# Kernel optimization log

Hardware: AMD Instinct MI355X
Metric: run time of the kernel (lower is better)

## Reference

```python
import jax, jax.numpy as jnp
import numpy as np

B, S, D = 1, 2048, 4096
H, KV, HD = 32, 8, 128
REP = H // KV            # 4, GQA repeat factor
THETA = 500000.0
NEG = -1e9               # stand-in for -inf in additive causal mask


def _rope(x, cos, sin):
    # x: [B,S,h,HD]; complex rotation on interleaved (even,odd) pairs,
    # matching torch.view_as_complex on [..., HD/2, 2]
    xr, xi = x[..., 0::2], x[..., 1::2]
    c = cos[None, :, None, :]
    s = sin[None, :, None, :]
    out_r = xr * c - xi * s
    out_i = xr * s + xi * c
    return jnp.stack([out_r, out_i], axis=-1).reshape(x.shape)


def setup_inputs() -> dict:
    key = jax.random.key(0)
    ks = jax.random.split(key, 6)
    x = jax.random.normal(ks[0], (B, S, D), dtype=jnp.float32)
    # torch nn.Linear weights are [out, in]
    sc = 1.0 / np.sqrt(D)
    wq = jax.random.normal(ks[1], (H * HD, D), dtype=jnp.float32) * sc
    wk = jax.random.normal(ks[2], (KV * HD, D), dtype=jnp.float32) * sc
    wv = jax.random.normal(ks[3], (KV * HD, D), dtype=jnp.float32) * sc
    wo = jax.random.normal(ks[4], (D, H * HD), dtype=jnp.float32) * sc
    # RoPE freqs_cis = exp(i * t * theta_f), stored as cos/sin [S, HD/2]
    freqs = 1.0 / (THETA ** (jnp.arange(0, HD, 2, dtype=jnp.float32) / HD))
    ang = jnp.outer(jnp.arange(S, dtype=jnp.float32), freqs)
    cos, sin = jnp.cos(ang), jnp.sin(ang)
    cache = jnp.zeros((2, B, S, KV, HD), dtype=jnp.float32)
    mask = jnp.where(jnp.tril(jnp.ones((S, S), dtype=bool)), 0.0, NEG).astype(jnp.float32)
    return {"x": x, "wq": wq, "wk": wk, "wv": wv, "wo": wo,
            "cos": cos, "sin": sin, "cache": cache, "mask": mask,
            "start_pos": 0}


def reference(x, wq, wk, wv, wo, cos, sin, cache, mask, start_pos):
    b, s, _ = x.shape
    xq = (x @ wq.T).reshape(b, s, H, HD)
    xk = (x @ wk.T).reshape(b, s, KV, HD)
    xv = (x @ wv.T).reshape(b, s, KV, HD)
    xq = _rope(xq, cos, sin)
    xk = _rope(xk, cos, sin)
    # functional KV-cache write
    cache = cache.at[0, :b, start_pos:start_pos + s].set(xk)
    cache = cache.at[1, :b, start_pos:start_pos + s].set(xv)
    keys = cache[0, :b, :start_pos + s]    # [b,T,KV,HD]
    values = cache[1, :b, :start_pos + s]  # [b,T,KV,HD]
    # GQA: head h = kv*REP + r (repeat_interleave ordering)
    q = xq.reshape(b, s, KV, REP, HD)
    scores = jnp.einsum('bskrd,btkd->bkrst', q, keys) / jnp.sqrt(jnp.float32(HD))
    scores = scores + mask[None, None, None]           # [b,KV,REP,s,T]
    p = jax.nn.softmax(scores.astype(jnp.float32), axis=-1).astype(x.dtype)
    out = jnp.einsum('bkrst,btkd->bskrd', p, values).reshape(b, s, H * HD)
    return out @ wo.T
```

## Files before the change

kernel.cpp:

```cpp
#include <hip/hip_runtime.h>
#include <stdint.h>

typedef __bf16 bf16_8 __attribute__((ext_vector_type(8)));
typedef __bf16 bf16_4 __attribute__((ext_vector_type(4)));
typedef float  f32x4  __attribute__((ext_vector_type(4)));

#define B_  1
#define S_  2048
#define D_  4096
#define H_  32
#define KV_ 8
#define HD_ 128

__device__ inline void gload_lds16(const void* g, void* l) {
  __builtin_amdgcn_global_load_lds((const __attribute__((address_space(1))) void*)g,
                                   (__attribute__((address_space(3))) void*)l, 16, 0, 0);
}

__global__ __launch_bounds__(256) void cvt_all(const float* __restrict__ x,
                                               const float* __restrict__ wq,
                                               const float* __restrict__ wk,
                                               const float* __restrict__ wv,
                                               const float* __restrict__ wo,
                                               __bf16* __restrict__ dst) {
  int i = blockIdx.x * 256 + threadIdx.x;
  const float* s;
  int j = i;
  if (j < 2097152) s = x;
  else if ((j -= 2097152) < 4194304) s = wq;
  else if ((j -= 4194304) < 1048576) s = wk;
  else if ((j -= 1048576) < 1048576) s = wv;
  else { j -= 1048576; s = wo; }
  float4 v = ((const float4*)s)[j];
  bf16_4 o = { (__bf16)v.x, (__bf16)v.y, (__bf16)v.z, (__bf16)v.w };
  ((bf16_4*)dst)[i] = o;
}

__global__ __launch_bounds__(256) void gemm_qkv(const __bf16* __restrict__ xb,
                                                const __bf16* __restrict__ wqb,
                                                const __bf16* __restrict__ wkb,
                                                const __bf16* __restrict__ wvb,
                                                const float* __restrict__ cosT,
                                                const float* __restrict__ sinT,
                                                __bf16* __restrict__ Qb,
                                                __bf16* __restrict__ Kb,
                                                __bf16* __restrict__ Vt) {
  __shared__ __bf16 As[128 * 32];
  __shared__ __bf16 Bs[128 * 32];
  const int nb = blockIdx.x, mb = blockIdx.y;
  const __bf16* W; int wrow0;
  if (nb < 32)      { W = wqb; wrow0 = nb * 128; }
  else if (nb < 40) { W = wkb; wrow0 = (nb - 32) * 128; }
  else              { W = wvb; wrow0 = (nb - 40) * 128; }
  const int tid = threadIdx.x, lane = tid & 63, wv = tid >> 6;
  const int wm = wv >> 1, wn = wv & 1;
  const int srow = lane >> 2, scol = (lane & 3) * 8;

  const __bf16* Ag0 = xb + (size_t)(mb * 128 + 2 * wv * 16 + srow) * D_ + scol;
  const __bf16* Bg0 = W  + (size_t)(wrow0 + 2 * wv * 16 + srow) * D_ + scol;
  __bf16* Al = As + 2 * wv * 512;
  __bf16* Bl = Bs + 2 * wv * 512;

  const f32x4 zv = {0.f, 0.f, 0.f, 0.f};
  f32x4 acc[4][4];
#pragma unroll
  for (int i = 0; i < 4; ++i)
#pragma unroll
    for (int j = 0; j < 4; ++j) acc[i][j] = zv;

  for (int k0 = 0; k0 < D_; k0 += 32) {
    gload_lds16(Ag0 + k0, Al);
    gload_lds16(Ag0 + (size_t)16 * D_ + k0, Al + 512);
    gload_lds16(Bg0 + k0, Bl);
    gload_lds16(Bg0 + (size_t)16 * D_ + k0, Bl + 512);
    __syncthreads();
    bf16_8 af[4], bfr[4];
#pragma unroll
    for (int i = 0; i < 4; ++i)
      af[i] = *(const bf16_8*)&As[(wm * 64 + i * 16 + (lane & 15)) * 32 + (lane >> 4) * 8];
#pragma unroll
    for (int j = 0; j < 4; ++j)
      bfr[j] = *(const bf16_8*)&Bs[(wn * 64 + j * 16 + (lane & 15)) * 32 + (lane >> 4) * 8];
#pragma unroll
    for (int i = 0; i < 4; ++i)
#pragma unroll
      for (int j = 0; j < 4; ++j)
        acc[i][j] = __builtin_amdgcn_mfma_f32_16x16x32_bf16(af[i], bfr[j], acc[i][j], 0, 0, 0);
    __syncthreads();
  }

#pragma unroll
  for (int i = 0; i < 4; ++i) {
    int row0 = mb * 128 + wm * 64 + i * 16 + (lane >> 4) * 4;
#pragma unroll
    for (int j = 0; j < 4; ++j) {
      int cl = wn * 64 + j * 16 + (lane & 15);
      if (nb < 40) {
        int f = cl >> 1;
        float sgn = (cl & 1) ? 1.f : -1.f;
        f32x4 v = acc[i][j];
        float o[4];
#pragma unroll
        for (int r = 0; r < 4; ++r) {
          float p = __shfl_xor(v[r], 1);
          float c = cosT[(size_t)(row0 + r) * 64 + f];
          float s = sinT[(size_t)(row0 + r) * 64 + f];
          o[r] = v[r] * c + sgn * p * s;
        }
        if (nb < 32) {
          int colg = nb * 128 + cl;
#pragma unroll
          for (int r = 0; r < 4; ++r)
            Qb[(size_t)(row0 + r) * D_ + colg] = (__bf16)o[r];
        } else {
          int colg = (nb - 32) * 128 + cl;
#pragma unroll
          for (int r = 0; r < 4; ++r)
            Kb[(size_t)(row0 + r) * 1024 + colg] = (__bf16)o[r];
        }
      } else {
        int colg = (nb - 40) * 128 + cl;
        bf16_4 pv = { (__bf16)acc[i][j][0], (__bf16)acc[i][j][1],
                      (__bf16)acc[i][j][2], (__bf16)acc[i][j][3] };
        *(bf16_4*)&Vt[(size_t)colg * S_ + row0] = pv;
      }
    }
  }
}

__global__ __launch_bounds__(256) void gemm_out(const __bf16* __restrict__ Ob,
                                                const __bf16* __restrict__ wob,
                                                float* __restrict__ Of) {
  __shared__ __bf16 As[128 * 32];
  __shared__ __bf16 Bs[128 * 32];
  const int nb = blockIdx.x, mb = blockIdx.y;
  const int tid = threadIdx.x, lane = tid & 63, wv = tid >> 6;
  const int wm = wv >> 1, wn = wv & 1;
  const int srow = lane >> 2, scol = (lane & 3) * 8;

  const __bf16* Ag0 = Ob  + (size_t)(mb * 128 + 2 * wv * 16 + srow) * D_ + scol;
  const __bf16* Bg0 = wob + (size_t)(nb * 128 + 2 * wv * 16 + srow) * D_ + scol;
  __bf16* Al = As + 2 * wv * 512;
  __bf16* Bl = Bs + 2 * wv * 512;

  const f32x4 zv = {0.f, 0.f, 0.f, 0.f};
  f32x4 acc[4][4];
#pragma unroll
  for (int i = 0; i < 4; ++i)
#pragma unroll
    for (int j = 0; j < 4; ++j) acc[i][j] = zv;

  for (int k0 = 0; k0 < D_; k0 += 32) {
    gload_lds16(Ag0 + k0, Al);
    gload_lds16(Ag0 + (size_t)16 * D_ + k0, Al + 512);
    gload_lds16(Bg0 + k0, Bl);
    gload_lds16(Bg0 + (size_t)16 * D_ + k0, Bl + 512);
    __syncthreads();
    bf16_8 af[4], bfr[4];
#pragma unroll
    for (int i = 0; i < 4; ++i)
      af[i] = *(const bf16_8*)&As[(wm * 64 + i * 16 + (lane & 15)) * 32 + (lane >> 4) * 8];
#pragma unroll
    for (int j = 0; j < 4; ++j)
      bfr[j] = *(const bf16_8*)&Bs[(wn * 64 + j * 16 + (lane & 15)) * 32 + (lane >> 4) * 8];
#pragma unroll
    for (int i = 0; i < 4; ++i)
#pragma unroll
      for (int j = 0; j < 4; ++j)
        acc[i][j] = __builtin_amdgcn_mfma_f32_16x16x32_bf16(af[i], bfr[j], acc[i][j], 0, 0, 0);
    __syncthreads();
  }

#pragma unroll
  for (int i = 0; i < 4; ++i) {
    int row0 = mb * 128 + wm * 64 + i * 16 + (lane >> 4) * 4;
#pragma unroll
    for (int j = 0; j < 4; ++j) {
      int colg = nb * 128 + wn * 64 + j * 16 + (lane & 15);
#pragma unroll
      for (int r = 0; r < 4; ++r)
        Of[(size_t)(row0 + r) * D_ + colg] = acc[i][j][r];
    }
  }
}

#define COMPUTE_TILE(ACC, MR, LR, AQ, QB0, DOMASK, KSB, VSB)                       \
  {                                                                                \
    f32x4 sfr_[4];                                                                 \
    __builtin_amdgcn_s_setprio(1);                                                 \
    _Pragma("unroll")                                                              \
    for (int nf = 0; nf < 4; ++nf) {                                               \
      f32x4 c_ = zv;                                                               \
      _Pragma("unroll")                                                            \
      for (int ks = 0; ks < 4; ++ks) {                                             \
        int n_ = nf * 16 + (lane & 15);                                            \
        int bo_ = (n_ * 256 + (ks * 32 + (lane >> 4) * 8) * 2) ^ ((n_ & 7) << 4);  \
        bf16_8 bk_ = *(const bf16_8*)((char*)(KSB) + bo_);                         \
        c_ = __builtin_amdgcn_mfma_f32_16x16x32_bf16(bk_, AQ[ks], c_, 0, 0, 0);    \
      }                                                                            \
      sfr_[nf] = c_;                                                               \
    }                                                                              \
    __builtin_amdgcn_s_setprio(0);                                                 \
    const int myq_ = (QB0) + w * 16 + (lane & 15);                                 \
    float pmn_[4];                                                                 \
    _Pragma("unroll")                                                              \
    for (int nf = 0; nf < 4; ++nf) {                                               \
      float t_ = -3e38f;                                                           \
      _Pragma("unroll")                                                            \
      for (int r = 0; r < 4; ++r) {                                                \
        int kcol_ = kb * 64 + nf * 16 + (lane >> 4) * 4 + r;                       \
        float v_ = sfr_[nf][r];                                                    \
        if ((DOMASK) && kcol_ > myq_) v_ = -1e9f;                                  \
        sfr_[nf][r] = v_;                                                          \
        t_ = fmaxf(t_, v_);                                                        \
      }                                                                            \
      pmn_[nf] = t_;                                                               \
    }                                                                              \
    float pm_ = fmaxf(fmaxf(pmn_[0], pmn_[1]), fmaxf(pmn_[2], pmn_[3]));           \
    pm_ = fmaxf(pm_, __shfl_xor(pm_, 16));                                         \
    pm_ = fmaxf(pm_, __shfl_xor(pm_, 32));                                         \
    if (!__all(pm_ <= MR + 8.f)) {                                                 \
      float mn_ = fmaxf(MR, pm_);                                                  \
      float rs_ = __expf(MR - mn_);                                                \
      MR = mn_;                                                                    \
      LR *= rs_;                                                                   \
      float rsb_[4];                                                               \
      _Pragma("unroll")                                                            \
      for (int r = 0; r < 4; ++r)                                                  \
        rsb_[r] = __shfl(rs_, (lane & 48) | ((lane >> 4) * 4 + r));                \
      _Pragma("unroll")                                                            \
      for (int d = 0; d < 8; ++d)                                                  \
        _Pragma("unroll")                                                          \
        for (int r = 0; r < 4; ++r) ACC[d][r] *= rsb_[r];                          \
    }                                                                              \
    float psn_[4];                                                                 \
    _Pragma("unroll")                                                              \
    for (int nf = 0; nf < 4; ++nf) {                                               \
      bf16_4 pk_;                                                                  \
      float t_ = 0.f;                                                              \
      _Pragma("unroll")                                                            \
      for (int r = 0; r < 4; ++r) {                                                \
        float p_ = __expf(sfr_[nf][r] - MR);                                       \
        t_ += p_;                                                                  \
        pk_[r] = (__bf16)p_;                                                       \
      }                                                                            \
      psn_[nf] = t_;                                                               \
      int bo_ = ((lane & 15) * 128 + nf * 32 + (lane >> 4) * 8) ^                  \
                (((lane & 15) & 7) << 4);                                          \
      *(bf16_4*)((char*)(&Ps[w][0]) + bo_) = pk_;                                  \
    }                                                                              \
    float ps_ = (psn_[0] + psn_[1]) + (psn_[2] + psn_[3]);                         \
    ps_ += __shfl_xor(ps_, 16);                                                    \
    ps_ += __shfl_xor(ps_, 32);                                                    \
    LR += ps_;                                                                     \
    bf16_8 ap_[2];                                                                 \
    _Pragma("unroll")                                                              \
    for (int ks = 0; ks < 2; ++ks) {                                               \
      int bo_ = ((lane & 15) * 128 + (ks * 32 + (lane >> 4) * 8) * 2) ^            \
                (((lane & 15) & 7) << 4);                                          \
      ap_[ks] = *(const bf16_8*)((char*)(&Ps[w][0]) + bo_);                        \
    }                                                                              \
    __builtin_amdgcn_s_setprio(1);                                                 \
    _Pragma("unroll")                                                              \
    for (int d = 0; d < 8; ++d) {                                                  \
      _Pragma("unroll")                                                            \
      for (int ks = 0; ks < 2; ++ks) {                                             \
        int dr_ = d * 16 + (lane & 15);                                            \
        int bo_ = (dr_ * 128 + (ks * 32 + (lane >> 4) * 8) * 2) ^ ((dr_ & 7) << 4);\
        bf16_8 bv_ = *(const bf16_8*)((char*)(VSB) + bo_);                         \
        ACC[d] = __builtin_amdgcn_mfma_f32_16x16x32_bf16(ap_[ks], bv_, ACC[d], 0, 0, 0); \
      }                                                                            \
    }                                                                              \
    __builtin_amdgcn_s_setprio(0);                                                 \
  }

__global__ __launch_bounds__(256) void attn_k(const __bf16* __restrict__ Qb,
                                              const __bf16* __restrict__ Kb,
                                              const __bf16* __restrict__ Vt,
                                              __bf16* __restrict__ Ob) {
  __shared__ __bf16 Ks[2][64 * 128];
  __shared__ __bf16 Vs[2][128 * 64];
  __shared__ __bf16 Ps[4][16 * 64];
  const int bid = blockIdx.x;
  const int kvh = bid & 7;
  const int j   = bid >> 3;
  const int h   = kvh * 4 + (j & 3);
  const int x   = j >> 2;
  const int qlo = x, qhi = 31 - x;
  const int tid = threadIdx.x, lane = tid & 63, w = tid >> 6;

  const float sc = 0.08838834764831845f;

  bf16_8 aq0[4], aq1[4];
#pragma unroll
  for (int ks = 0; ks < 4; ++ks) {
    int rr = w * 16 + (lane & 15);
    int cc = h * 128 + ks * 32 + (lane >> 4) * 8;
    bf16_8 t0 = *(const bf16_8*)&Qb[(size_t)(qlo * 64 + rr) * D_ + cc];
    bf16_8 t1 = *(const bf16_8*)&Qb[(size_t)(qhi * 64 + rr) * D_ + cc];
#pragma unroll
    for (int e = 0; e < 8; ++e) {
      aq0[ks][e] = (__bf16)((float)t0[e] * sc);
      aq1[ks][e] = (__bf16)((float)t1[e] * sc);
    }
  }

  const f32x4 zv = {0.f, 0.f, 0.f, 0.f};
  f32x4 accO0[8], accO1[8];
#pragma unroll
  for (int d = 0; d < 8; ++d) { accO0[d] = zv; accO1[d] = zv; }
  float mr0 = -3e38f, lr0 = 0.f, mr1 = -3e38f, lr1 = 0.f;

#define KSTAGE(BUF, KB)                                                            \
  {                                                                                \
    _Pragma("unroll")                                                              \
    for (int u = 0; u < 4; ++u) {                                                  \
      int chunk = (u * 4 + w) * 64 + lane;                                         \
      int row = chunk >> 4, p8 = chunk & 15;                                       \
      gload_lds16(&Kb[(size_t)((KB) * 64 + row) * 1024 + kvh * 128 + (p8 ^ (row & 7)) * 8], \
                  &Ks[BUF][(u * 4 + w) * 512]);                                    \
    }                                                                              \
    _Pragma("unroll")                                                              \
    for (int u = 0; u < 4; ++u) {                                                  \
      int chunk = (u * 4 + w) * 64 + lane;                                         \
      int vr = chunk >> 3, p8 = chunk & 7;                                         \
      gload_lds16(&Vt[(size_t)(kvh * 128 + vr) * S_ + (KB) * 64 + (p8 ^ (vr & 7)) * 8], \
                  &Vs[BUF][(u * 4 + w) * 512]);                                    \
    }                                                                              \
  }

  KSTAGE(0, 0);
  asm volatile("s_waitcnt vmcnt(0)" ::: "memory");
  __syncthreads();

  for (int kb = 0; kb <= qhi; ++kb) {
    const int cur = kb & 1;
    if (kb < qhi) KSTAGE(cur ^ 1, kb + 1);
    const __bf16* ksb = &Ks[cur][0];
    const __bf16* vsb = &Vs[cur][0];
    COMPUTE_TILE(accO1, mr1, lr1, aq1, qhi * 64, (kb == qhi), ksb, vsb);
    if (kb <= qlo) COMPUTE_TILE(accO0, mr0, lr0, aq0, qlo * 64, (kb == qlo), ksb, vsb);
    if (kb < qhi) {
      asm volatile("s_waitcnt vmcnt(0)" ::: "memory");
      __syncthreads();
    }
  }

  float inv0[4], inv1[4];
#pragma unroll
  for (int r = 0; r < 4; ++r) {
    int src = (lane & 48) | ((lane >> 4) * 4 + r);
    inv0[r] = 1.0f / __shfl(lr0, src);
    inv1[r] = 1.0f / __shfl(lr1, src);
  }
#pragma unroll
  for (int d = 0; d < 8; ++d) {
#pragma unroll
    for (int r = 0; r < 4; ++r) {
      size_t rl = (size_t)(qlo * 64 + w * 16 + (lane >> 4) * 4 + r);
      size_t rh = (size_t)(qhi * 64 + w * 16 + (lane >> 4) * 4 + r);
      int cc = h * 128 + d * 16 + (lane & 15);
      Ob[rl * D_ + cc] = (__bf16)(accO0[d][r] * inv0[r]);
      Ob[rh * D_ + cc] = (__bf16)(accO1[d][r] * inv1[r]);
    }
  }
}

extern "C" void kernel_launch(void* const* d_in, const int* in_sizes, int n_in,
                              void* d_out, int out_size, void* d_ws, size_t ws_size,
                              hipStream_t stream) {
  const float* x    = (const float*)d_in[0];
  const float* wq   = (const float*)d_in[1];
  const float* wk   = (const float*)d_in[2];
  const float* wv   = (const float*)d_in[3];
  const float* wo   = (const float*)d_in[4];
  const float* cosT = (const float*)d_in[5];
  const float* sinT = (const float*)d_in[6];
  float* out = (float*)d_out;
  char* ws = (char*)d_ws;

  __bf16* xb  = (__bf16*)(ws + 0);
  __bf16* wqb = (__bf16*)(ws + 16777216);
  __bf16* wkb = (__bf16*)(ws + 50331648);
  __bf16* wvb = (__bf16*)(ws + 58720256);
  __bf16* wob = (__bf16*)(ws + 67108864);
  __bf16* Qb  = (__bf16*)(ws + 100663296);
  __bf16* Kb  = (__bf16*)(ws + 117440512);
  __bf16* Vt  = (__bf16*)(ws + 121634816);
  __bf16* Ob  = xb;

  cvt_all<<<49152, 256, 0, stream>>>(x, wq, wk, wv, wo, xb);

  gemm_qkv<<<dim3(48, 16), 256, 0, stream>>>(xb, wqb, wkb, wvb, cosT, sinT, Qb, Kb, Vt);

  attn_k<<<512, 256, 0, stream>>>(Qb, Kb, Vt, Ob);

  gemm_out<<<dim3(32, 16), 256, 0, stream>>>(Ob, wob, out);
}
```

Baseline: 374.9 us.

## Widen GEMM K-tile to 64 with XOR-swizzled LDS layout

Both projection GEMMs now stage 64-wide K slices per iteration instead of 32. This halves the number of barrier pairs and brings two MFMA k-steps per sync. The LDS tiles are stored with an XOR swizzle on 16-byte chunks, applied on the global-to-LDS load and on the fragment reads, to avoid bank conflicts with 128-byte rows. LDS use doubles to 32KB per block, which may limit occupancy, and there is still no double buffering.

```diff
diff --git a/kernel.cpp b/kernel.cpp
--- a/kernel.cpp
+++ b/kernel.cpp
@@ -36,6 +36,18 @@
   ((bf16_4*)dst)[i] = o;
 }
 
+#define GSTAGE64(GBASE, LDSBASE)                                                   \
+  _Pragma("unroll")                                                                \
+  for (int u = 0; u < 4; ++u) {                                                    \
+    int row_ = u * 32 + wv * 8 + (lane >> 3);                                      \
+    int pc_ = (lane & 7) ^ (lane >> 3);                                            \
+    gload_lds16((GBASE) + (size_t)row_ * D_ + k0 + pc_ * 8,                        \
+                (LDSBASE) + (u * 32 + wv * 8) * 64);                               \
+  }
+#define FRAG64(LDSBASE, ROW, KS)                                                   \
+  (*(const bf16_8*)((const char*)(LDSBASE) +                                       \
+      (((ROW) * 128 + (KS) * 64 + (lane >> 4) * 16) ^ (((ROW) & 7) << 4))))
+
 __global__ __launch_bounds__(256) void gemm_qkv(const __bf16* __restrict__ xb,
                                                 const __bf16* __restrict__ wqb,
                                                 const __bf16* __restrict__ wkb,
@@ -45,8 +57,8 @@
                                                 __bf16* __restrict__ Qb,
                                                 __bf16* __restrict__ Kb,
                                                 __bf16* __restrict__ Vt) {
-  __shared__ __bf16 As[128 * 32];
-  __shared__ __bf16 Bs[128 * 32];
+  __shared__ __bf16 As[128 * 64];
+  __shared__ __bf16 Bs[128 * 64];
   const int nb = blockIdx.x, mb = blockIdx.y;
   const __bf16* W; int wrow0;
   if (nb < 32)      { W = wqb; wrow0 = nb * 128; }
@@ -54,12 +66,9 @@
   else              { W = wvb; wrow0 = (nb - 40) * 128; }
   const int tid = threadIdx.x, lane = tid & 63, wv = tid >> 6;
   const int wm = wv >> 1, wn = wv & 1;
-  const int srow = lane >> 2, scol = (lane & 3) * 8;
-
-  const __bf16* Ag0 = xb + (size_t)(mb * 128 + 2 * wv * 16 + srow) * D_ + scol;
-  const __bf16* Bg0 = W  + (size_t)(wrow0 + 2 * wv * 16 + srow) * D_ + scol;
-  __bf16* Al = As + 2 * wv * 512;
-  __bf16* Bl = Bs + 2 * wv * 512;
+
+  const __bf16* Ag = xb + (size_t)(mb * 128) * D_;
+  const __bf16* Bg = W + (size_t)wrow0 * D_;
 
   const f32x4 zv = {0.f, 0.f, 0.f, 0.f};
   f32x4 acc[4][4];
@@ -68,24 +77,25 @@
 #pragma unroll
     for (int j = 0; j < 4; ++j) acc[i][j] = zv;
 
-  for (int k0 = 0; k0 < D_; k0 += 32) {
-    gload_lds16(Ag0 + k0, Al);
-    gload_lds16(Ag0 + (size_t)16 * D_ + k0, Al + 512);
-    gload_lds16(Bg0 + k0, Bl);
-    gload_lds16(Bg0 + (size_t)16 * D_ + k0, Bl + 512);
+  for (int k0 = 0; k0 < D_; k0 += 64) {
+    GSTAGE64(Ag, As);
+    GSTAGE64(Bg, Bs);
     __syncthreads();
-    bf16_8 af[4], bfr[4];
-#pragma unroll
-    for (int i = 0; i < 4; ++i)
-      af[i] = *(const bf16_8*)&As[(wm * 64 + i * 16 + (lane & 15)) * 32 + (lane >> 4) * 8];
-#pragma unroll
-    for (int j = 0; j < 4; ++j)
-      bfr[j] = *(const bf16_8*)&Bs[(wn * 64 + j * 16 + (lane & 15)) * 32 + (lane >> 4) * 8];
-#pragma unroll
-    for (int i = 0; i < 4; ++i)
+#pragma unroll
+    for (int ks = 0; ks < 2; ++ks) {
+      bf16_8 af[4], bfr[4];
+#pragma unroll
+      for (int i = 0; i < 4; ++i)
+        af[i] = FRAG64(As, wm * 64 + i * 16 + (lane & 15), ks);
 #pragma unroll
       for (int j = 0; j < 4; ++j)
-        acc[i][j] = __builtin_amdgcn_mfma_f32_16x16x32_bf16(af[i], bfr[j], acc[i][j], 0, 0, 0);
+        bfr[j] = FRAG64(Bs, wn * 64 + j * 16 + (lane & 15), ks);
+#pragma unroll
+      for (int i = 0; i < 4; ++i)
+#pragma unroll
+        for (int j = 0; j < 4; ++j)
+          acc[i][j] = __builtin_amdgcn_mfma_f32_16x16x32_bf16(af[i], bfr[j], acc[i][j], 0, 0, 0);
+    }
     __syncthreads();
   }
 
@@ -131,17 +141,14 @@
 __global__ __launch_bounds__(256) void gemm_out(const __bf16* __restrict__ Ob,
                                                 const __bf16* __restrict__ wob,
                                                 float* __restrict__ Of) {
-  __shared__ __bf16 As[128 * 32];
-  __shared__ __bf16 Bs[128 * 32];
+  __shared__ __bf16 As[128 * 64];
+  __shared__ __bf16 Bs[128 * 64];
   const int nb = blockIdx.x, mb = blockIdx.y;
   const int tid = threadIdx.x, lane = tid & 63, wv = tid >> 6;
   const int wm = wv >> 1, wn = wv & 1;
-  const int srow = lane >> 2, scol = (lane & 3) * 8;
-
-  const __bf16* Ag0 = Ob  + (size_t)(mb * 128 + 2 * wv * 16 + srow) * D_ + scol;
-  const __bf16* Bg0 = wob + (size_t)(nb * 128 + 2 * wv * 16 + srow) * D_ + scol;
-  __bf16* Al = As + 2 * wv * 512;
-  __bf16* Bl = Bs + 2 * wv * 512;
+
+  const __bf16* Ag = Ob + (size_t)(mb * 128) * D_;
+  const __bf16* Bg = wob + (size_t)(nb * 128) * D_;
 
   const f32x4 zv = {0.f, 0.f, 0.f, 0.f};
   f32x4 acc[4][4];
@@ -150,24 +157,25 @@
 #pragma unroll
     for (int j = 0; j < 4; ++j) acc[i][j] = zv;
 
-  for (int k0 = 0; k0 < D_; k0 += 32) {
-    gload_lds16(Ag0 + k0, Al);
-    gload_lds16(Ag0 + (size_t)16 * D_ + k0, Al + 512);
-    gload_lds16(Bg0 + k0, Bl);
-    gload_lds16(Bg0 + (size_t)16 * D_ + k0, Bl + 512);
+  for (int k0 = 0; k0 < D_; k0 += 64) {
+    GSTAGE64(Ag, As);
+    GSTAGE64(Bg, Bs);
     __syncthreads();
-    bf16_8 af[4], bfr[4];
-#pragma unroll
-    for (int i = 0; i < 4; ++i)
-      af[i] = *(const bf16_8*)&As[(wm * 64 + i * 16 + (lane & 15)) * 32 + (lane >> 4) * 8];
-#pragma unroll
-    for (int j = 0; j < 4; ++j)
-      bfr[j] = *(const bf16_8*)&Bs[(wn * 64 + j * 16 + (lane & 15)) * 32 + (lane >> 4) * 8];
-#pragma unroll
-    for (int i = 0; i < 4; ++i)
+#pragma unroll
+    for (int ks = 0; ks < 2; ++ks) {
+      bf16_8 af[4], bfr[4];
+#pragma unroll
+      for (int i = 0; i < 4; ++i)
+        af[i] = FRAG64(As, wm * 64 + i * 16 + (lane & 15), ks);
 #pragma unroll
       for (int j = 0; j < 4; ++j)
-        acc[i][j] = __builtin_amdgcn_mfma_f32_16x16x32_bf16(af[i], bfr[j], acc[i][j], 0, 0, 0);
+        bfr[j] = FRAG64(Bs, wn * 64 + j * 16 + (lane & 15), ks);
+#pragma unroll
+      for (int i = 0; i < 4; ++i)
+#pragma unroll
+        for (int j = 0; j < 4; ++j)
+          acc[i][j] = __builtin_amdgcn_mfma_f32_16x16x32_bf16(af[i], bfr[j], acc[i][j], 0, 0, 0);
+    }
     __syncthreads();
   }
 
```

New measurement: 386.4 us. 3.1% more time.

## Split attention block into 8 waves, one per query tile of the pair

Applied to the files above, without the earlier changes.

The attention kernel previously had 4 waves each process both the low and high query tiles of a causally balanced pair. It now launches 512 threads, with waves 0-3 handling the high tile and waves 4-7 the low tile, so each wave holds one accumulator set. K/V staging is spread over all 8 waves. This halves per-wave register pressure and adds more waves per CU. The trade-off is that the low-tile waves sit idle after their causal limit while the high-tile waves continue, and the block syncs still include them.

```diff
diff --git a/kernel.cpp b/kernel.cpp
--- a/kernel.cpp
+++ b/kernel.cpp
@@ -201,7 +201,7 @@
       sfr_[nf] = c_;                                                               \
     }                                                                              \
     __builtin_amdgcn_s_setprio(0);                                                 \
-    const int myq_ = (QB0) + w * 16 + (lane & 15);                                 \
+    const int myq_ = (QB0) + w4 * 16 + (lane & 15);                                \
     float pmn_[4];                                                                 \
     _Pragma("unroll")                                                              \
     for (int nf = 0; nf < 4; ++nf) {                                               \
@@ -247,7 +247,7 @@
       psn_[nf] = t_;                                                               \
       int bo_ = ((lane & 15) * 128 + nf * 32 + (lane >> 4) * 8) ^                  \
                 (((lane & 15) & 7) << 4);                                          \
-      *(bf16_4*)((char*)(&Ps[w][0]) + bo_) = pk_;                                  \
+      *(bf16_4*)((char*)(&Ps[wid][0]) + bo_) = pk_;                                \
     }                                                                              \
     float ps_ = (psn_[0] + psn_[1]) + (psn_[2] + psn_[3]);                         \
     ps_ += __shfl_xor(ps_, 16);                                                    \
@@ -258,7 +258,7 @@
     for (int ks = 0; ks < 2; ++ks) {                                               \
       int bo_ = ((lane & 15) * 128 + (ks * 32 + (lane >> 4) * 8) * 2) ^            \
                 (((lane & 15) & 7) << 4);                                          \
-      ap_[ks] = *(const bf16_8*)((char*)(&Ps[w][0]) + bo_);                        \
+      ap_[ks] = *(const bf16_8*)((char*)(&Ps[wid][0]) + bo_);                      \
     }                                                                              \
     __builtin_amdgcn_s_setprio(1);                                                 \
     _Pragma("unroll")                                                              \
@@ -274,58 +274,56 @@
     __builtin_amdgcn_s_setprio(0);                                                 \
   }
 
-__global__ __launch_bounds__(256) void attn_k(const __bf16* __restrict__ Qb,
-                                              const __bf16* __restrict__ Kb,
-                                              const __bf16* __restrict__ Vt,
-                                              __bf16* __restrict__ Ob) {
+__global__ __launch_bounds__(512, 4) void attn_k(const __bf16* __restrict__ Qb,
+                                                 const __bf16* __restrict__ Kb,
+                                                 const __bf16* __restrict__ Vt,
+                                                 __bf16* __restrict__ Ob) {
   __shared__ __bf16 Ks[2][64 * 128];
   __shared__ __bf16 Vs[2][128 * 64];
-  __shared__ __bf16 Ps[4][16 * 64];
+  __shared__ __bf16 Ps[8][16 * 64];
   const int bid = blockIdx.x;
   const int kvh = bid & 7;
   const int j   = bid >> 3;
   const int h   = kvh * 4 + (j & 3);
   const int x   = j >> 2;
   const int qlo = x, qhi = 31 - x;
-  const int tid = threadIdx.x, lane = tid & 63, w = tid >> 6;
+  const int tid = threadIdx.x, lane = tid & 63, wid = tid >> 6;
+  const int w4 = wid & 3;
+  const int qt = (wid < 4) ? qhi : qlo;
 
   const float sc = 0.08838834764831845f;
 
-  bf16_8 aq0[4], aq1[4];
+  bf16_8 aq[4];
 #pragma unroll
   for (int ks = 0; ks < 4; ++ks) {
-    int rr = w * 16 + (lane & 15);
+    int rr = qt * 64 + w4 * 16 + (lane & 15);
     int cc = h * 128 + ks * 32 + (lane >> 4) * 8;
-    bf16_8 t0 = *(const bf16_8*)&Qb[(size_t)(qlo * 64 + rr) * D_ + cc];
-    bf16_8 t1 = *(const bf16_8*)&Qb[(size_t)(qhi * 64 + rr) * D_ + cc];
-#pragma unroll
-    for (int e = 0; e < 8; ++e) {
-      aq0[ks][e] = (__bf16)((float)t0[e] * sc);
-      aq1[ks][e] = (__bf16)((float)t1[e] * sc);
-    }
+    bf16_8 t = *(const bf16_8*)&Qb[(size_t)rr * D_ + cc];
+#pragma unroll
+    for (int e = 0; e < 8; ++e) aq[ks][e] = (__bf16)((float)t[e] * sc);
   }
 
   const f32x4 zv = {0.f, 0.f, 0.f, 0.f};
-  f32x4 accO0[8], accO1[8];
-#pragma unroll
-  for (int d = 0; d < 8; ++d) { accO0[d] = zv; accO1[d] = zv; }
-  float mr0 = -3e38f, lr0 = 0.f, mr1 = -3e38f, lr1 = 0.f;
+  f32x4 acc[8];
+#pragma unroll
+  for (int d = 0; d < 8; ++d) acc[d] = zv;
+  float mr = -3e38f, lr = 0.f;
 
 #define KSTAGE(BUF, KB)                                                            \
   {                                                                                \
     _Pragma("unroll")                                                              \
-    for (int u = 0; u < 4; ++u) {                                                  \
-      int chunk = (u * 4 + w) * 64 + lane;                                         \
+    for (int u = 0; u < 2; ++u) {                                                  \
+      int chunk = (u * 8 + wid) * 64 + lane;                                       \
       int row = chunk >> 4, p8 = chunk & 15;                                       \
       gload_lds16(&Kb[(size_t)((KB) * 64 + row) * 1024 + kvh * 128 + (p8 ^ (row & 7)) * 8], \
-                  &Ks[BUF][(u * 4 + w) * 512]);                                    \
-    }                                                                              \
-    _Pragma("unroll")                                                              \
-    for (int u = 0; u < 4; ++u) {                                                  \
-      int chunk = (u * 4 + w) * 64 + lane;                                         \
+                  &Ks[BUF][(u * 8 + wid) * 512]);                                  \
+    }                                                                              \
+    _Pragma("unroll")                                                              \
+    for (int u = 0; u < 2; ++u) {                                                  \
+      int chunk = (u * 8 + wid) * 64 + lane;                                       \
       int vr = chunk >> 3, p8 = chunk & 7;                                         \
       gload_lds16(&Vt[(size_t)(kvh * 128 + vr) * S_ + (KB) * 64 + (p8 ^ (vr & 7)) * 8], \
-                  &Vs[BUF][(u * 4 + w) * 512]);                                    \
+                  &Vs[BUF][(u * 8 + wid) * 512]);                                  \
     }                                                                              \
   }
 
@@ -338,30 +336,23 @@
     if (kb < qhi) KSTAGE(cur ^ 1, kb + 1);
     const __bf16* ksb = &Ks[cur][0];
     const __bf16* vsb = &Vs[cur][0];
-    COMPUTE_TILE(accO1, mr1, lr1, aq1, qhi * 64, (kb == qhi), ksb, vsb);
-    if (kb <= qlo) COMPUTE_TILE(accO0, mr0, lr0, aq0, qlo * 64, (kb == qlo), ksb, vsb);
+    if (kb <= qt) COMPUTE_TILE(acc, mr, lr, aq, qt * 64, (kb == qt), ksb, vsb);
     if (kb < qhi) {
       asm volatile("s_waitcnt vmcnt(0)" ::: "memory");
       __syncthreads();
     }
   }
 
-  float inv0[4], inv1[4];
-#pragma unroll
-  for (int r = 0; r < 4; ++r) {
-    int src = (lane & 48) | ((lane >> 4) * 4 + r);
-    inv0[r] = 1.0f / __shfl(lr0, src);
-    inv1[r] = 1.0f / __shfl(lr1, src);
-  }
+  float inv[4];
+#pragma unroll
+  for (int r = 0; r < 4; ++r)
+    inv[r] = 1.0f / __shfl(lr, (lane & 48) | ((lane >> 4) * 4 + r));
 #pragma unroll
   for (int d = 0; d < 8; ++d) {
 #pragma unroll
     for (int r = 0; r < 4; ++r) {
-      size_t rl = (size_t)(qlo * 64 + w * 16 + (lane >> 4) * 4 + r);
-      size_t rh = (size_t)(qhi * 64 + w * 16 + (lane >> 4) * 4 + r);
-      int cc = h * 128 + d * 16 + (lane & 15);
-      Ob[rl * D_ + cc] = (__bf16)(accO0[d][r] * inv0[r]);
-      Ob[rh * D_ + cc] = (__bf16)(accO1[d][r] * inv1[r]);
+      size_t row = (size_t)(qt * 64 + w4 * 16 + (lane >> 4) * 4 + r);
+      Ob[row * D_ + h * 128 + d * 16 + (lane & 15)] = (__bf16)(acc[d][r] * inv[r]);
     }
   }
 }
@@ -393,7 +384,7 @@
 
   gemm_qkv<<<dim3(48, 16), 256, 0, stream>>>(xb, wqb, wkb, wvb, cosT, sinT, Qb, Kb, Vt);
 
-  attn_k<<<512, 256, 0, stream>>>(Qb, Kb, Vt, Ob);
+  attn_k<<<512, 512, 0, stream>>>(Qb, Kb, Vt, Ob);
 
   gemm_out<<<dim3(32, 16), 256, 0, stream>>>(Ob, wob, out);
 }
```

New measurement: 372.5 us. About the same (-0.6%).
